# Kernel tuning notes

Measured on AMD Instinct MI355X. Metric: run time of the kernel, lower is better.

The kernel has to match this reference:

```python
import jax, jax.numpy as jnp
import numpy as np
from jax import lax

D_MODEL = 512
D_FIBER = 32
D_CONTROL = 64
MOMENTUM = 0.9


def setup_inputs() -> dict:
    key = jax.random.key(0)
    ks = jax.random.split(key, 7)
    B, S = 8, 4096
    hidden = jax.random.normal(ks[0], (B, S, D_MODEL), dtype=jnp.float32)
    # fiber_proj: Linear(d_model -> d_fiber)
    w_fiber = jax.random.normal(ks[1], (D_MODEL, D_FIBER), dtype=jnp.float32) / np.sqrt(D_MODEL)
    b_fiber = jnp.zeros((D_FIBER,), dtype=jnp.float32)
    # predictor: Linear(d_model+d_fiber -> d_control), GELU, Linear(d_control -> 1), Softplus
    w1 = jax.random.normal(ks[2], (D_MODEL + D_FIBER, D_CONTROL), dtype=jnp.float32) / np.sqrt(D_MODEL + D_FIBER)
    b1 = jnp.zeros((D_CONTROL,), dtype=jnp.float32)
    # nn.init.normal_(weight, std=0.01), zero bias for the last linear
    w2 = 0.01 * jax.random.normal(ks[3], (D_CONTROL, 1), dtype=jnp.float32)
    b2 = jnp.zeros((1,), dtype=jnp.float32)
    lambda_gate = jnp.asarray(1.0, dtype=jnp.float32)
    return {"hidden": hidden, "w_fiber": w_fiber, "b_fiber": b_fiber,
            "w1": w1, "b1": b1, "w2": w2, "b2": b2, "lambda_gate": lambda_gate}


def _ema_scan(delta_h, momentum):
    # field_t = momentum * field_{t-1} + (1-momentum) * delta_h_t, field_{-1}=0.
    # Same math as the original full-length causal conv1d (Toeplitz) form,
    # computed in O(S log S) via an associative scan.
    a = jnp.full_like(delta_h, momentum)
    b = (1.0 - momentum) * delta_h

    def combine(c1, c2):
        a1, b1 = c1
        a2, b2 = c2
        return (a1 * a2, a2 * b1 + b2)

    _, field = lax.associative_scan(combine, (a, b), axis=1)
    return field


def reference(hidden, w_fiber, b_fiber, w1, b1, w2, b2, lambda_gate):
    # hidden: [B, S, D]
    fiber = hidden @ w_fiber + b_fiber                      # [B, S, d_fiber]
    combined = jnp.concatenate([hidden, fiber], axis=-1)    # [B, S, D+d_fiber]
    h = jax.nn.gelu(combined @ w1 + b1, approximate=False)  # [B, S, d_control]
    delta_h = jax.nn.softplus((h @ w2 + b2).squeeze(-1))    # [B, S]
    delta_h = jnp.clip(delta_h, 0.0, 1.0)
    field = _ema_scan(delta_h, MOMENTUM)                    # [B, S]
    field = jnp.clip(field, 0.0, 10.0)
    gate = jax.nn.sigmoid(-lambda_gate * field)             # [B, S]
    return (gate, field, delta_h, fiber)
```

## Files before the change

### kernel.cpp

```cpp
#include <hip/hip_runtime.h>
#include <hip/hip_bf16.h>


#define NTOK  32768
#define SEQ   4096
#define DM    512
#define NC    96
#define TB    64
#define KC    128
#define LROW  136

typedef short bf16x8 __attribute__((ext_vector_type(8)));
typedef float f32x4  __attribute__((ext_vector_type(4)));

__device__ __forceinline__ unsigned short f2bf(float f) {
    __hip_bfloat16 h = __float2bfloat16(f);
    return *reinterpret_cast<unsigned short*>(&h);
}

__device__ __forceinline__ bf16x8 cvt8(float4 u, float4 v) {
    bf16x8 r;
    r[0] = (short)f2bf(u.x); r[1] = (short)f2bf(u.y);
    r[2] = (short)f2bf(u.z); r[3] = (short)f2bf(u.w);
    r[4] = (short)f2bf(v.x); r[5] = (short)f2bf(v.y);
    r[6] = (short)f2bf(v.z); r[7] = (short)f2bf(v.w);
    return r;
}

__global__ __launch_bounds__(256)
void prep_kernel(const float* __restrict__ wf,
                 const float* __restrict__ bfb,
                 const float* __restrict__ w1,
                 const float* __restrict__ b1,
                 unsigned short* __restrict__ Wt,
                 float* __restrict__ bc)
{
    int idx = blockIdx.x * 256 + threadIdx.x;
    if (idx < NC * DM) {
        int n = idx >> 9, k = idx & 511;
        float v;
        if (n < 32) {
            v = wf[k * 32 + n];
        } else {
            int c = n - 32;
            v = w1[k * 64 + c];
            const float4* wfr = (const float4*)(wf + k * 32);
#pragma unroll
            for (int f4 = 0; f4 < 8; ++f4) {
                float4 u = wfr[f4];
                v = fmaf(u.x, w1[(512 + f4 * 4 + 0) * 64 + c], v);
                v = fmaf(u.y, w1[(512 + f4 * 4 + 1) * 64 + c], v);
                v = fmaf(u.z, w1[(512 + f4 * 4 + 2) * 64 + c], v);
                v = fmaf(u.w, w1[(512 + f4 * 4 + 3) * 64 + c], v);
            }
        }
        Wt[idx] = f2bf(v);
    }
    if (idx < NC) {
        float v;
        if (idx < 32) {
            v = bfb[idx];
        } else {
            int c = idx - 32;
            v = b1[c];
            for (int f = 0; f < 32; ++f)
                v = fmaf(bfb[f], w1[(512 + f) * 64 + c], v);
        }
        bc[idx] = v;
    }
}

__global__ __launch_bounds__(256, 2)
void fused_gemm_kernel(const float* __restrict__ hidden,
                       const unsigned short* __restrict__ Wt,
                       const float* __restrict__ bc,
                       const float* __restrict__ w2,
                       const float* __restrict__ b2,
                       float* __restrict__ out_delta,
                       float* __restrict__ out_fiber)
{
    __shared__ unsigned short b_lds[NC * LROW];

    const int tid  = threadIdx.x;
    const int wave = tid >> 6;
    const int lane = tid & 63;
    const int quad = lane >> 4;
    const int l15  = lane & 15;
    const int tok0 = blockIdx.x * TB;

    const float* arow = hidden + (size_t)(tok0 + wave * 16 + l15) * DM + quad * 8;

    f32x4 acc[6];
#pragma unroll
    for (int t = 0; t < 6; ++t) acc[t] = (f32x4){0.f, 0.f, 0.f, 0.f};

#pragma unroll 1
    for (int kc = 0; kc < DM; kc += KC) {
        bf16x8 breg[6];
#pragma unroll
        for (int it = 0; it < 6; ++it) {
            int v = it * 256 + tid;
            breg[it] = *(const bf16x8*)(Wt + (v >> 4) * DM + kc + (v & 15) * 8);
        }
        float4 a[8];
#pragma unroll
        for (int ks = 0; ks < 4; ++ks) {
            const float* ap = arow + kc + ks * 32;
            a[2 * ks]     = *(const float4*)ap;
            a[2 * ks + 1] = *(const float4*)(ap + 4);
        }
#pragma unroll
        for (int it = 0; it < 6; ++it) {
            int v = it * 256 + tid;
            *(bf16x8*)&b_lds[(v >> 4) * LROW + (v & 15) * 8] = breg[it];
        }
        __syncthreads();

        bf16x8 af[4];
#pragma unroll
        for (int ks = 0; ks < 4; ++ks) af[ks] = cvt8(a[2 * ks], a[2 * ks + 1]);

#pragma unroll
        for (int ks = 0; ks < 4; ++ks) {
#pragma unroll
            for (int t = 0; t < 6; ++t) {
                bf16x8 bfv = *(const bf16x8*)&b_lds[(t * 16 + l15) * LROW + ks * 32 + quad * 8];
                acc[t] = __builtin_amdgcn_mfma_f32_16x16x32_bf16(af[ks], bfv, acc[t], 0, 0, 0);
            }
        }
        __syncthreads();
    }

    const int mbase = tok0 + wave * 16 + quad * 4;

#pragma unroll
    for (int t = 0; t < 2; ++t) {
        int col = t * 16 + l15;
        float bias = bc[col];
#pragma unroll
        for (int r = 0; r < 4; ++r)
            out_fiber[(size_t)(mbase + r) * 32 + col] = acc[t][r] + bias;
    }

    float p0 = 0.f, p1 = 0.f, p2 = 0.f, p3 = 0.f;
#pragma unroll
    for (int t = 2; t < 6; ++t) {
        int c = (t - 2) * 16 + l15;
        float bias = bc[32 + c];
        float w2v  = w2[c];
        float x, g;
        x = acc[t][0] + bias; g = 0.5f * x * (1.f + erff(x * 0.70710678118f)); p0 = fmaf(g, w2v, p0);
        x = acc[t][1] + bias; g = 0.5f * x * (1.f + erff(x * 0.70710678118f)); p1 = fmaf(g, w2v, p1);
        x = acc[t][2] + bias; g = 0.5f * x * (1.f + erff(x * 0.70710678118f)); p2 = fmaf(g, w2v, p2);
        x = acc[t][3] + bias; g = 0.5f * x * (1.f + erff(x * 0.70710678118f)); p3 = fmaf(g, w2v, p3);
    }
#pragma unroll
    for (int m = 1; m <= 8; m <<= 1) {
        p0 += __shfl_xor(p0, m);
        p1 += __shfl_xor(p1, m);
        p2 += __shfl_xor(p2, m);
        p3 += __shfl_xor(p3, m);
    }
    if (l15 < 4) {
        float pv = (l15 == 0) ? p0 : (l15 == 1) ? p1 : (l15 == 2) ? p2 : p3;
        float s = pv + b2[0];
        float d = (s > 0.f) ? s + log1pf(expf(-s)) : log1pf(expf(s));
        d = fminf(fmaxf(d, 0.f), 1.f);
        out_delta[mbase + l15] = d;
    }
}

__global__ __launch_bounds__(256)
void scan_kernel(const float* __restrict__ delta,
                 const float* __restrict__ lam,
                 float* __restrict__ out_gate,
                 float* __restrict__ out_field)
{
    __shared__ float lds_d[384];
    const int b     = blockIdx.x >> 4;
    const int chunk = blockIdx.x & 15;
    const int s0    = chunk * 256;
    const int tid   = threadIdx.x;

    for (int v = tid; v < 384; v += 256) {
        int s = s0 - 128 + v;
        lds_d[v] = (s >= 0) ? delta[b * SEQ + s] : 0.f;
    }
    __syncthreads();

    const int base = 128 + tid;
    const float r4 = 0.6561f;
    float w0 = 0.1f, w1v = 0.09f, w2v = 0.081f, w3v = 0.0729f;
    float p0 = 0.f, p1 = 0.f, p2 = 0.f, p3 = 0.f;
#pragma unroll
    for (int j = 0; j < 128; j += 4) {
        p0 = fmaf(w0,  lds_d[base - j],     p0); w0  *= r4;
        p1 = fmaf(w1v, lds_d[base - j - 1], p1); w1v *= r4;
        p2 = fmaf(w2v, lds_d[base - j - 2], p2); w2v *= r4;
        p3 = fmaf(w3v, lds_d[base - j - 3], p3); w3v *= r4;
    }
    float field = fminf(fmaxf((p0 + p1) + (p2 + p3), 0.f), 10.f);

    float gate = 1.f / (1.f + expf(lam[0] * field));
    int t = b * SEQ + s0 + tid;
    out_field[t] = field;
    out_gate[t]  = gate;
}

extern "C" void kernel_launch(void* const* d_in, const int* in_sizes, int n_in,
                              void* d_out, int out_size, void* d_ws, size_t ws_size,
                              hipStream_t stream)
{
    const float* hidden = (const float*)d_in[0];
    const float* wf     = (const float*)d_in[1];
    const float* bfb    = (const float*)d_in[2];
    const float* w1     = (const float*)d_in[3];
    const float* b1     = (const float*)d_in[4];
    const float* w2     = (const float*)d_in[5];
    const float* b2     = (const float*)d_in[6];
    const float* lam    = (const float*)d_in[7];
    float* out = (float*)d_out;
    float* out_gate  = out;
    float* out_field = out + NTOK;
    float* out_delta = out + 2 * NTOK;
    float* out_fiber = out + 3 * NTOK;

    unsigned short* Wt = (unsigned short*)d_ws;
    float* bc          = (float*)((char*)d_ws + NC * DM * 2);

    hipLaunchKernelGGL(prep_kernel, dim3((NC * DM + 255) / 256), dim3(256), 0, stream,
                       wf, bfb, w1, b1, Wt, bc);
    hipLaunchKernelGGL(fused_gemm_kernel, dim3(NTOK / TB), dim3(256), 0, stream,
                       hidden, Wt, bc, w2, b2, out_delta, out_fiber);
    hipLaunchKernelGGL(scan_kernel, dim3(128), dim3(256), 0, stream,
                       out_delta, lam, out_gate, out_field);
}
```

Before: 120.2 us.

## Split GEMM K loop into two halves with register-staged prefetch of weights

Replaces the four-iteration K loop over 128-wide chunks with two 256-wide halves. The second half of the weight tile is loaded into registers while the first half's MFMAs run, then written to LDS. Occupancy hint is raised to 3 blocks per CU. LDS usage grows to about 50KB per block and register pressure rises from the 12-deep staging array, which may limit the occupancy actually reached. Activation loads now happen per k-step inside the compute loop instead of being batched up front.

After: 119.2 us. About the same (-0.8%).

```diff
diff --git a/kernel.cpp b/kernel.cpp
--- a/kernel.cpp
+++ b/kernel.cpp
@@ -7,8 +7,8 @@
 #define DM    512
 #define NC    96
 #define TB    64
-#define KC    128
-#define LROW  136
+#define KC    256
+#define LROW  264
 
 typedef short bf16x8 __attribute__((ext_vector_type(8)));
 typedef float f32x4  __attribute__((ext_vector_type(4)));
@@ -70,7 +70,7 @@
     }
 }
 
-__global__ __launch_bounds__(256, 2)
+__global__ __launch_bounds__(256, 3)
 void fused_gemm_kernel(const float* __restrict__ hidden,
                        const unsigned short* __restrict__ Wt,
                        const float* __restrict__ bc,
@@ -94,41 +94,55 @@
 #pragma unroll
     for (int t = 0; t < 6; ++t) acc[t] = (f32x4){0.f, 0.f, 0.f, 0.f};
 
-#pragma unroll 1
-    for (int kc = 0; kc < DM; kc += KC) {
-        bf16x8 breg[6];
-#pragma unroll
-        for (int it = 0; it < 6; ++it) {
-            int v = it * 256 + tid;
-            breg[it] = *(const bf16x8*)(Wt + (v >> 4) * DM + kc + (v & 15) * 8);
-        }
-        float4 a[8];
-#pragma unroll
-        for (int ks = 0; ks < 4; ++ks) {
-            const float* ap = arow + kc + ks * 32;
-            a[2 * ks]     = *(const float4*)ap;
-            a[2 * ks + 1] = *(const float4*)(ap + 4);
-        }
-#pragma unroll
-        for (int it = 0; it < 6; ++it) {
-            int v = it * 256 + tid;
-            *(bf16x8*)&b_lds[(v >> 4) * LROW + (v & 15) * 8] = breg[it];
-        }
-        __syncthreads();
-
-        bf16x8 af[4];
-#pragma unroll
-        for (int ks = 0; ks < 4; ++ks) af[ks] = cvt8(a[2 * ks], a[2 * ks + 1]);
-
-#pragma unroll
-        for (int ks = 0; ks < 4; ++ks) {
-#pragma unroll
-            for (int t = 0; t < 6; ++t) {
-                bf16x8 bfv = *(const bf16x8*)&b_lds[(t * 16 + l15) * LROW + ks * 32 + quad * 8];
-                acc[t] = __builtin_amdgcn_mfma_f32_16x16x32_bf16(af[ks], bfv, acc[t], 0, 0, 0);
-            }
-        }
-        __syncthreads();
+#pragma unroll
+    for (int it = 0; it < 12; ++it) {
+        int v   = it * 256 + tid;
+        int row = v >> 5;
+        int c8  = v & 31;
+        bf16x8 u = *(const bf16x8*)(Wt + row * DM + c8 * 8);
+        *(bf16x8*)&b_lds[row * LROW + c8 * 8] = u;
+    }
+    __syncthreads();
+
+    bf16x8 bstage[12];
+#pragma unroll
+    for (int it = 0; it < 12; ++it) {
+        int v   = it * 256 + tid;
+        bstage[it] = *(const bf16x8*)(Wt + (v >> 5) * DM + KC + (v & 31) * 8);
+    }
+
+#pragma unroll
+    for (int ks = 0; ks < 8; ++ks) {
+        const float* ap = arow + ks * 32;
+        float4 a0 = *(const float4*)ap;
+        float4 a1 = *(const float4*)(ap + 4);
+        bf16x8 af = cvt8(a0, a1);
+#pragma unroll
+        for (int t = 0; t < 6; ++t) {
+            bf16x8 bfv = *(const bf16x8*)&b_lds[(t * 16 + l15) * LROW + ks * 32 + quad * 8];
+            acc[t] = __builtin_amdgcn_mfma_f32_16x16x32_bf16(af, bfv, acc[t], 0, 0, 0);
+        }
+    }
+    __syncthreads();
+
+#pragma unroll
+    for (int it = 0; it < 12; ++it) {
+        int v = it * 256 + tid;
+        *(bf16x8*)&b_lds[(v >> 5) * LROW + (v & 31) * 8] = bstage[it];
+    }
+    __syncthreads();
+
+#pragma unroll
+    for (int ks = 0; ks < 8; ++ks) {
+        const float* ap = arow + KC + ks * 32;
+        float4 a0 = *(const float4*)ap;
+        float4 a1 = *(const float4*)(ap + 4);
+        bf16x8 af = cvt8(a0, a1);
+#pragma unroll
+        for (int t = 0; t < 6; ++t) {
+            bf16x8 bfv = *(const bf16x8*)&b_lds[(t * 16 + l15) * LROW + ks * 32 + quad * 8];
+            acc[t] = __builtin_amdgcn_mfma_f32_16x16x32_bf16(af, bfv, acc[t], 0, 0, 0);
+        }
     }
 
     const int mbase = tok0 + wave * 16 + quad * 4;
```
